# Kernel optimization log

Hardware: AMD Instinct MI355X
Metric: run time of the kernel (lower is better)

The kernel has to match this reference:

```python
import jax, jax.numpy as jnp
import numpy as np

B, S, D, H = 4, 2048, 2048, 16
HD = D // H  # 128
THETA = 10000.0


def setup_inputs() -> dict:
    key = jax.random.key(0)
    k1, k2, k3 = jax.random.split(key, 3)
    x = jax.random.normal(k1, (B, S, D), dtype=jnp.float32)
    wqkv = jax.random.normal(k2, (3 * D, D), dtype=jnp.float32) * (1.0 / np.sqrt(D))
    wo = jax.random.normal(k3, (D, D), dtype=jnp.float32) * (1.0 / np.sqrt(D))
    return {"x": x, "wqkv": wqkv, "wo": wo}


def _rotate_half(t):
    t1 = t[..., : t.shape[-1] // 2]
    t2 = t[..., t.shape[-1] // 2 :]
    return jnp.concatenate([-t2, t1], axis=-1)


def reference(x, wqkv, wo):
    b, s, d = x.shape
    h, hd = H, HD
    # fused QKV projection (Linear without bias: x @ W^T)
    qkv = jnp.einsum("bsd,ed->bse", x, wqkv).reshape(b, s, 3, h, hd)
    xq, xk, xv = qkv[:, :, 0], qkv[:, :, 1], qkv[:, :, 2]

    # RoPE tables (start_pos = 0)
    inv_freq = 1.0 / (THETA ** (jnp.arange(0, hd, 2, dtype=jnp.float32) / hd))
    t = jnp.arange(s, dtype=jnp.float32)
    freqs = jnp.outer(t, inv_freq)  # [s, hd/2]
    cos = jnp.concatenate([jnp.cos(freqs)] * 2, axis=-1).reshape(1, s, 1, hd)
    sin = jnp.concatenate([jnp.sin(freqs)] * 2, axis=-1).reshape(1, s, 1, hd)

    xq = xq * cos + _rotate_half(xq) * sin
    xk = xk * cos + _rotate_half(xk) * sin

    # causal SDPA (kv_cache is None, seq_len > 1)
    scale = 1.0 / np.sqrt(hd)
    scores = jnp.einsum("bqhd,bkhd->bhqk", xq, xk) * scale
    causal = jnp.tril(jnp.ones((s, s), dtype=bool))
    scores = jnp.where(causal, scores, jnp.finfo(scores.dtype).min)
    attn = jax.nn.softmax(scores, axis=-1)
    out = jnp.einsum("bhqk,bkhd->bqhd", attn, xv).reshape(b, s, d)
    return jnp.einsum("bsd,od->bso", out, wo)
```

## Files before the change

kernel.cpp:

```cpp
#include <hip/hip_runtime.h>

typedef unsigned short u16;
typedef unsigned int u32;
typedef __bf16 bf16x8 __attribute__((ext_vector_type(8)));
typedef float f32x4 __attribute__((ext_vector_type(4)));

#define S_LEN 2048
#define NH 16
#define HD 128

#define AS1 __attribute__((address_space(1)))
#define AS3 __attribute__((address_space(3)))

__device__ __forceinline__ u16 f2bf(float x) {
  u32 u = __builtin_bit_cast(u32, x);
  u32 r = u + 0x7FFFu + ((u >> 16) & 1u);
  return (u16)(r >> 16);
}
__device__ __forceinline__ float bf2f(u16 b) {
  return __builtin_bit_cast(float, (u32)b << 16);
}

__global__ void cvt_f32_bf16(const float* __restrict__ in, u16* __restrict__ out, int n4) {
  int i = blockIdx.x * 256 + threadIdx.x;
  if (i >= n4) return;
  float4 v = ((const float4*)in)[i];
  ushort4 o;
  o.x = f2bf(v.x); o.y = f2bf(v.y); o.z = f2bf(v.z); o.w = f2bf(v.w);
  ((ushort4*)out)[i] = o;
}

__global__ void build_tab(float* __restrict__ tab) {
  int t = blockIdx.x * 256 + threadIdx.x;
  int s = t >> 6, j = t & 63;
  float inv = exp2f(-(float)j * 0.20762050593045083f);
  float ang = (float)s * inv;
  tab[t] = cosf(ang);
  tab[131072 + t] = sinf(ang);
}

__device__ __forceinline__ void storeC(u16* p, float v) { *p = f2bf(v); }
__device__ __forceinline__ void storeC(float* p, float v) { *p = v; }

template <typename OutT>
__global__ __launch_bounds__(512, 2) void gemm_bt5(const u16* __restrict__ A, const u16* __restrict__ B,
                                                   OutT* __restrict__ C, int M, int N, int K, int nbx) {
  __shared__ alignas(16) u16 LDS[65536];
  char* lds = (char*)LDS;
  const int tid = threadIdx.x;
  const int lane = tid & 63;
  const int w = tid >> 6;
  const int wr = w >> 2, wc = w & 3;
  const int g = lane >> 4, c = lane & 15;

  const int nwg = gridDim.x;
  const int id = blockIdx.x;
  const int sw = (id & 7) * (nwg >> 3) + (id >> 3);
  const int bx = sw % nbx, by = sw / nbx;
  const size_t rowBase = (size_t)by * 256;
  const size_t colBase = (size_t)bx * 256;

  const int half = w & 1;
  const int sub = (w >> 1) & 3;
  const size_t ldb = (size_t)K * 2;
  const int srow = lane >> 3;
  const int soff = ((lane & 7) ^ srow) << 4;
  const char* ApS = (const char*)A + (rowBase + half * 128 + srow) * ldb + soff;
  const char* BpS = (const char*)B + (colBase + half * 128 + srow) * ldb + soff;

  auto stA = [&](int u, int blk) {
    const int r0 = blk * 32 + sub * 8;
    const int dst = ((u & 1) * 2 + half) * 16384 + r0 * 128;
    __builtin_amdgcn_global_load_lds((const AS1 void*)(ApS + (size_t)r0 * ldb + (size_t)u * 128),
                                     (AS3 void*)(lds + dst), 16, 0, 0);
  };
  auto stB = [&](int u, int jj) {
    const int r0 = (sub * 4 + jj) * 8;
    const int dst = 65536 + ((u & 1) * 2 + half) * 16384 + r0 * 128;
    __builtin_amdgcn_global_load_lds((const AS1 void*)(BpS + (size_t)r0 * ldb + (size_t)u * 128),
                                     (AS3 void*)(lds + dst), 16, 0, 0);
  };

  const int swz = (c & 7) << 4;
  auto rdA = [&](int bA, int mi, int kk) -> bf16x8 {
    return *(const bf16x8*)(lds + bA + mi * 2048 + c * 128 + ((kk * 64 + g * 16) ^ swz));
  };
  auto rdB = [&](int bB, int n, int kk) -> bf16x8 {
    return *(const bf16x8*)(lds + bB + n * 2048 + c * 128 + ((kk * 64 + g * 16) ^ swz));
  };

  f32x4 acc[8][4];
#pragma unroll
  for (int m = 0; m < 8; ++m)
#pragma unroll
    for (int n = 0; n < 4; ++n) acc[m][n] = f32x4{0.f, 0.f, 0.f, 0.f};

  bf16x8 bf_[4][2];
  auto mfmaPair = [&](int mi, bf16x8 ak0, bf16x8 ak1) {
#pragma unroll
    for (int n = 0; n < 4; ++n) {
      acc[mi][n] = __builtin_amdgcn_mfma_f32_16x16x32_bf16(ak0, bf_[n][0], acc[mi][n], 0, 0, 0);
      acc[mi][n] = __builtin_amdgcn_mfma_f32_16x16x32_bf16(ak1, bf_[n][1], acc[mi][n], 0, 0, 0);
    }
  };

  const int NT = K >> 6;

#pragma unroll
  for (int b = 0; b < 4; ++b) stA(0, b);
#pragma unroll
  for (int j = 0; j < 4; ++j) stB(0, j);
#pragma unroll
  for (int b = 0; b < 4; ++b) stA(1, b);
#pragma unroll
  for (int j = 0; j < 4; ++j) stB(1, j);
  asm volatile("s_waitcnt vmcnt(8)" ::: "memory");
  __builtin_amdgcn_s_barrier();

#pragma unroll 1
  for (int t = 0; t < NT; ++t) {
    const int bA = (t & 1) * 32768 + wr * 16384;
    const int bB = 65536 + (t & 1) * 32768 + (wc >> 1) * 16384 + (wc & 1) * 8192;
    bf16x8 a00, a01, a10, a11;
    a00 = rdA(bA, 0, 0); a01 = rdA(bA, 0, 1); a10 = rdA(bA, 1, 0); a11 = rdA(bA, 1, 1);
#pragma unroll
    for (int n = 0; n < 4; ++n) { bf_[n][0] = rdB(bB, n, 0); bf_[n][1] = rdB(bB, n, 1); }
    if (t >= 1 && t + 1 < NT) stA(t + 1, 3);
    __builtin_amdgcn_s_barrier();
    asm volatile("s_waitcnt lgkmcnt(0)" ::: "memory");
    __builtin_amdgcn_sched_barrier(0);
    __builtin_amdgcn_s_setprio(1);
    mfmaPair(0, a00, a01);
    mfmaPair(1, a10, a11);
    __builtin_amdgcn_s_setprio(0);
    __builtin_amdgcn_sched_barrier(0);
    __builtin_amdgcn_s_barrier();
    a00 = rdA(bA, 2, 0); a01 = rdA(bA, 2, 1); a10 = rdA(bA, 3, 0); a11 = rdA(bA, 3, 1);
    if (t + 2 < NT) { stA(t + 2, 0); stB(t + 2, 0); stB(t + 2, 1); }
    __builtin_amdgcn_s_barrier();
    asm volatile("s_waitcnt lgkmcnt(0)" ::: "memory");
    __builtin_amdgcn_sched_barrier(0);
    __builtin_amdgcn_s_setprio(1);
    mfmaPair(2, a00, a01);
    mfmaPair(3, a10, a11);
    __builtin_amdgcn_s_setprio(0);
    __builtin_amdgcn_sched_barrier(0);
    __builtin_amdgcn_s_barrier();
    a00 = rdA(bA, 4, 0); a01 = rdA(bA, 4, 1); a10 = rdA(bA, 5, 0); a11 = rdA(bA, 5, 1);
    if (t + 2 < NT) { stA(t + 2, 1); stB(t + 2, 2); stB(t + 2, 3); }
    __builtin_amdgcn_s_barrier();
    asm volatile("s_waitcnt lgkmcnt(0)" ::: "memory");
    __builtin_amdgcn_sched_barrier(0);
    __builtin_amdgcn_s_setprio(1);
    mfmaPair(4, a00, a01);
    mfmaPair(5, a10, a11);
    __builtin_amdgcn_s_setprio(0);
    __builtin_amdgcn_sched_barrier(0);
    __builtin_amdgcn_s_barrier();
    a00 = rdA(bA, 6, 0); a01 = rdA(bA, 6, 1); a10 = rdA(bA, 7, 0); a11 = rdA(bA, 7, 1);
    if (t + 2 < NT) stA(t + 2, 2);
    __builtin_amdgcn_s_barrier();
    asm volatile("s_waitcnt lgkmcnt(0)" ::: "memory");
    __builtin_amdgcn_sched_barrier(0);
    __builtin_amdgcn_s_setprio(1);
    mfmaPair(6, a00, a01);
    mfmaPair(7, a10, a11);
    __builtin_amdgcn_s_setprio(0);
    __builtin_amdgcn_sched_barrier(0);
    if (t + 2 < NT) { asm volatile("s_waitcnt vmcnt(7)" ::: "memory"); }
    else            { asm volatile("s_waitcnt vmcnt(0)" ::: "memory"); }
    __builtin_amdgcn_s_barrier();
  }

#pragma unroll
  for (int m = 0; m < 8; ++m)
#pragma unroll
    for (int n = 0; n < 4; ++n) {
      size_t row = rowBase + wr * 128 + m * 16 + g * 4;
      size_t col = colBase + wc * 64 + n * 16 + c;
#pragma unroll
      for (int r = 0; r < 4; ++r)
        storeC(&C[(row + r) * (size_t)N + col], acc[m][n][r]);
    }
}

__global__ void rope_qk(const u16* __restrict__ qkv, const float* __restrict__ tab,
                        u16* __restrict__ Q, u16* __restrict__ K) {
  int idx = blockIdx.x * 256 + threadIdx.x;
  int j = idx & 63;
  int s = (idx >> 6) & (S_LEN - 1);
  int h = (idx >> 17) & (NH - 1);
  int b = idx >> 21;
  float cs = tab[s * 64 + j];
  float sn = tab[131072 + s * 64 + j];
  size_t qbase = (((size_t)(b * S_LEN + s) * 3 + 0) * NH + h) * HD;
  size_t kbase = qbase + (size_t)NH * HD;
  size_t o = ((size_t)(b * NH + h) * S_LEN + s) * HD;
  float q1 = bf2f(qkv[qbase + j]),  q2 = bf2f(qkv[qbase + j + 64]);
  Q[o + j]      = f2bf(q1 * cs - q2 * sn);
  Q[o + j + 64] = f2bf(q2 * cs + q1 * sn);
  float k1 = bf2f(qkv[kbase + j]), k2 = bf2f(qkv[kbase + j + 64]);
  K[o + j]      = f2bf(k1 * cs - k2 * sn);
  K[o + j + 64] = f2bf(k2 * cs + k1 * sn);
}

__global__ void v_transpose(const u16* __restrict__ qkv, u16* __restrict__ Vt) {
  __shared__ u16 t[32][33];
  int bh = blockIdx.z;
  int s0 = blockIdx.x * 32;
  int d0 = blockIdx.y * 32;
  int b = bh >> 4, h = bh & 15;
  int col = threadIdx.x & 31;
  int row = threadIdx.x >> 5;
#pragma unroll
  for (int i = 0; i < 4; ++i) {
    int s = row + i * 8;
    t[s][col] = qkv[(((size_t)(b * S_LEN + s0 + s) * 3 + 2) * NH + h) * HD + d0 + col];
  }
  __syncthreads();
  size_t vb = ((size_t)bh * HD + d0) * S_LEN + s0;
#pragma unroll
  for (int i = 0; i < 4; ++i) {
    int d = row + i * 8;
    Vt[vb + (size_t)d * S_LEN + col] = t[col][d];
  }
}

__global__ __launch_bounds__(512, 4) void attn_fwd(const u16* __restrict__ Q, const u16* __restrict__ K,
                                                   const u16* __restrict__ Vt, u16* __restrict__ O) {
  __shared__ alignas(16) u16 Ks[2 * 64 * 128];
  __shared__ alignas(16) u16 Vs[2 * 128 * 64];
  __shared__ alignas(16) u16 Pl[8 * 16 * 64];
  const int tid = threadIdx.x;
  const int lane = tid & 63;
  const int w = tid >> 6;
  const int g = lane >> 4, c = lane & 15;
  const int bh = blockIdx.x;
  const int pair = blockIdx.y;
  const int b = bh >> 4, h = bh & 15;

  const u16* Qb = Q + (size_t)bh * S_LEN * HD;
  const u16* Kb = K + (size_t)bh * S_LEN * HD;
  const u16* Vb = Vt + (size_t)bh * HD * S_LEN;
  const float SL = 0.12751753f;
  const int swz = (c & 7) << 4;

  int ldsOff[2], srcK[2], srcV[2];
#pragma unroll
  for (int ii = 0; ii < 2; ++ii) {
    int p = (w * 2 + ii) * 1024 + lane * 16;
    ldsOff[ii] = p;
    int rk = p >> 8, ik = p & 255;
    srcK[ii] = rk * 256 + (ik ^ ((rk & 7) << 4));
    int rv = p >> 7, iv = p & 127;
    srcV[ii] = rv * (S_LEN * 2) + (iv ^ ((rv & 7) << 4));
  }
  int koff[4], voff[2];
#pragma unroll
  for (int kb = 0; kb < 4; ++kb) koff[kb] = (kb * 64 + g * 16) ^ swz;
  voff[0] = (g * 16) ^ swz;
  voff[1] = (64 + g * 16) ^ swz;
  int poff[4];
#pragma unroll
  for (int t = 0; t < 4; ++t) poff[t] = (t * 32 + g * 8) ^ swz;
  char* Pw = (char*)Pl + w * 2048;

#pragma unroll 1
  for (int ph = 0; ph < 2; ++ph) {
    const int sti = ph ? (15 - pair) : pair;
    const int qb0 = sti * 128;
    const int q0 = qb0 + w * 16;

    bf16x8 qf[4];
#pragma unroll
    for (int kb = 0; kb < 4; ++kb)
      qf[kb] = *(const bf16x8*)&Qb[(size_t)(q0 + c) * HD + kb * 32 + g * 8];

    f32x4 acc[8];
#pragma unroll
    for (int cb = 0; cb < 8; ++cb) acc[cb] = f32x4{0.f, 0.f, 0.f, 0.f};
    float m_i = -3e38f, l_i = 0.f;

    const int nsteps = sti * 2 + 2;
#pragma unroll
    for (int ii = 0; ii < 2; ++ii) {
      __builtin_amdgcn_global_load_lds((const AS1 void*)((const char*)Kb + srcK[ii]),
                                       (AS3 void*)((char*)Ks + ldsOff[ii] - lane * 16), 16, 0, 0);
      __builtin_amdgcn_global_load_lds((const AS1 void*)((const char*)Vb + srcV[ii]),
                                       (AS3 void*)((char*)Vs + ldsOff[ii] - lane * 16), 16, 0, 0);
    }
    __syncthreads();
    int cur = 0;

#pragma unroll 1
    for (int st = 0; st < nsteps; ++st) {
      const int kv0 = st << 6;
      if (st + 1 < nsteps) {
        const char* kbase = (const char*)Kb + (size_t)(kv0 + 64) * 256;
        const char* vbase = (const char*)Vb + (size_t)(kv0 + 64) * 2;
        const int nb = (cur ^ 1) * 16384;
#pragma unroll
        for (int ii = 0; ii < 2; ++ii) {
          __builtin_amdgcn_global_load_lds((const AS1 void*)(kbase + srcK[ii]),
                                           (AS3 void*)((char*)Ks + nb + ldsOff[ii] - lane * 16), 16, 0, 0);
          __builtin_amdgcn_global_load_lds((const AS1 void*)(vbase + srcV[ii]),
                                           (AS3 void*)((char*)Vs + nb + ldsOff[ii] - lane * 16), 16, 0, 0);
        }
      }
      if (kv0 < q0 + 16) {
        const char* Kt = (const char*)Ks + cur * 16384;
        const char* Vtl = (const char*)Vs + cur * 16384;
        f32x4 s[4];
#pragma unroll
        for (int t = 0; t < 4; ++t) s[t] = f32x4{0.f, 0.f, 0.f, 0.f};
#pragma unroll
        for (int t = 0; t < 4; ++t)
#pragma unroll
          for (int kb = 0; kb < 4; ++kb) {
            bf16x8 kf = *(const bf16x8*)(Kt + t * 4096 + c * 256 + koff[kb]);
            s[t] = __builtin_amdgcn_mfma_f32_16x16x32_bf16(kf, qf[kb], s[t], 0, 0, 0);
          }
        if (kv0 + 63 > q0) {
          const int lim = q0 + c - kv0 - 4 * g;
#pragma unroll
          for (int t = 0; t < 4; ++t)
#pragma unroll
            for (int r = 0; r < 4; ++r)
              s[t][r] = (16 * t + r <= lim) ? s[t][r] : -3e38f;
        }
        float mx = s[0][0];
#pragma unroll
        for (int t = 0; t < 4; ++t)
#pragma unroll
          for (int r = 0; r < 4; ++r) mx = fmaxf(mx, s[t][r]);
        mx = fmaxf(mx, __shfl_xor(mx, 16));
        mx = fmaxf(mx, __shfl_xor(mx, 32));
        const float mn = fmaxf(m_i, mx);
        const float alpha = exp2f((m_i - mn) * SL);
        float rs = 0.f;
#pragma unroll
        for (int t = 0; t < 4; ++t) {
          float p0 = exp2f((s[t][0] - mn) * SL);
          float p1 = exp2f((s[t][1] - mn) * SL);
          float p2 = exp2f((s[t][2] - mn) * SL);
          float p3 = exp2f((s[t][3] - mn) * SL);
          rs += (p0 + p1) + (p2 + p3);
          ushort4 pw;
          pw.x = f2bf(p0); pw.y = f2bf(p1); pw.z = f2bf(p2); pw.w = f2bf(p3);
          *(ushort4*)(Pw + c * 128 + poff[t]) = pw;
        }
        rs += __shfl_xor(rs, 16);
        rs += __shfl_xor(rs, 32);
        l_i = l_i * alpha + rs;
        m_i = mn;
        float ar[4];
#pragma unroll
        for (int r = 0; r < 4; ++r) ar[r] = __shfl(alpha, 4 * g + r);
#pragma unroll
        for (int cb = 0; cb < 8; ++cb)
#pragma unroll
          for (int r = 0; r < 4; ++r) acc[cb][r] *= ar[r];
        bf16x8 pa0 = *(const bf16x8*)(Pw + c * 128 + voff[0]);
        bf16x8 pa1 = *(const bf16x8*)(Pw + c * 128 + voff[1]);
#pragma unroll
        for (int cb = 0; cb < 8; ++cb) {
          bf16x8 vf0 = *(const bf16x8*)(Vtl + cb * 2048 + c * 128 + voff[0]);
          acc[cb] = __builtin_amdgcn_mfma_f32_16x16x32_bf16(pa0, vf0, acc[cb], 0, 0, 0);
          bf16x8 vf1 = *(const bf16x8*)(Vtl + cb * 2048 + c * 128 + voff[1]);
          acc[cb] = __builtin_amdgcn_mfma_f32_16x16x32_bf16(pa1, vf1, acc[cb], 0, 0, 0);
        }
      }
      __syncthreads();
      cur ^= 1;
    }
    float linv = 1.0f / l_i;
    float lr[4];
#pragma unroll
    for (int r = 0; r < 4; ++r) lr[r] = __shfl(linv, 4 * g + r);
#pragma unroll
    for (int cb = 0; cb < 8; ++cb)
#pragma unroll
      for (int r = 0; r < 4; ++r) {
        int q = q0 + 4 * g + r;
        O[(((size_t)b * S_LEN + q) * NH + h) * HD + cb * 16 + c] = f2bf(acc[cb][r] * lr[r]);
      }
  }
}

extern "C" void kernel_launch(void* const* d_in, const int* in_sizes, int n_in,
                              void* d_out, int out_size, void* d_ws, size_t ws_size,
                              hipStream_t stream) {
  const float* x    = (const float*)d_in[0];
  const float* wqkv = (const float*)d_in[1];
  const float* wo   = (const float*)d_in[2];
  float* out = (float*)d_out;
  char* ws = (char*)d_ws;

  u16*  xb    = (u16*)(ws + 0);
  u16*  wqkvb = (u16*)(ws + 33554432);
  float* tab  = (float*)(ws + 58720256);
  u16*  wob   = (u16*)(ws + 58720256);
  u16*  qkvb  = (u16*)(ws + 67108864);
  u16*  Vt    = (u16*)(ws + 167772160);
  u16*  attn  = (u16*)(ws + 0);
  u16*  Qr = (u16*)d_out;
  u16*  Kr = (u16*)d_out + 16777216;

  cvt_f32_bf16<<<16384, 256, 0, stream>>>(x, xb, 16777216 / 4);
  cvt_f32_bf16<<<12288, 256, 0, stream>>>(wqkv, wqkvb, 12582912 / 4);
  build_tab<<<512, 256, 0, stream>>>(tab);

  gemm_bt5<u16><<<768, 512, 0, stream>>>(xb, wqkvb, qkvb, 8192, 6144, 2048, 24);

  rope_qk<<<32768, 256, 0, stream>>>(qkvb, tab, Qr, Kr);
  v_transpose<<<dim3(64, 4, 64), 256, 0, stream>>>(qkvb, Vt);

  cvt_f32_bf16<<<4096, 256, 0, stream>>>(wo, wob, 4194304 / 4);

  attn_fwd<<<dim3(64, 8), 512, 0, stream>>>(Qr, Kr, Vt, attn);

  gemm_bt5<float><<<256, 512, 0, stream>>>(attn, wob, out, 8192, 2048, 2048, 8);
}
```

Measured before the change: 451.3 us.

## Double-buffer A fragments in registers to overlap LDS reads with MFMA

Restructures the GEMM inner loop so the A-operand LDS reads for the next pair of row-blocks are issued before the current MFMAs run, using two register sets (aP/aQ) and partial lgkmcnt waits. The first fragment set for the next K-tile is preloaded at the end of each iteration, and one barrier per phase is removed. This aims to hide LDS latency behind matrix work, at the cost of more VGPRs, which risks spills under the 512x2 launch bounds.

```diff
diff --git a/kernel.cpp b/kernel.cpp
--- a/kernel.cpp
+++ b/kernel.cpp
@@ -43,7 +43,7 @@
 __device__ __forceinline__ void storeC(float* p, float v) { *p = v; }
 
 template <typename OutT>
-__global__ __launch_bounds__(512, 2) void gemm_bt5(const u16* __restrict__ A, const u16* __restrict__ B,
+__global__ __launch_bounds__(512, 2) void gemm_bt6(const u16* __restrict__ A, const u16* __restrict__ B,
                                                    OutT* __restrict__ C, int M, int N, int K, int nbx) {
   __shared__ alignas(16) u16 LDS[65536];
   char* lds = (char*)LDS;
@@ -96,11 +96,24 @@
     for (int n = 0; n < 4; ++n) acc[m][n] = f32x4{0.f, 0.f, 0.f, 0.f};
 
   bf16x8 bf_[4][2];
-  auto mfmaPair = [&](int mi, bf16x8 ak0, bf16x8 ak1) {
+  bf16x8 aP[4], aQ[4];
+
+  auto loadA = [&](bf16x8 (&s)[4], int bA, int mi) {
+    s[0] = rdA(bA, mi, 0); s[1] = rdA(bA, mi, 1);
+    s[2] = rdA(bA, mi + 1, 0); s[3] = rdA(bA, mi + 1, 1);
+  };
+  auto loadR1 = [&](int bA, int bB) {
+    loadA(aP, bA, 0);
+#pragma unroll
+    for (int n = 0; n < 4; ++n) { bf_[n][0] = rdB(bB, n, 0); bf_[n][1] = rdB(bB, n, 1); }
+  };
+  auto MFMA2 = [&](int mi, bf16x8 (&s)[4]) {
 #pragma unroll
     for (int n = 0; n < 4; ++n) {
-      acc[mi][n] = __builtin_amdgcn_mfma_f32_16x16x32_bf16(ak0, bf_[n][0], acc[mi][n], 0, 0, 0);
-      acc[mi][n] = __builtin_amdgcn_mfma_f32_16x16x32_bf16(ak1, bf_[n][1], acc[mi][n], 0, 0, 0);
+      acc[mi][n]     = __builtin_amdgcn_mfma_f32_16x16x32_bf16(s[0], bf_[n][0], acc[mi][n], 0, 0, 0);
+      acc[mi][n]     = __builtin_amdgcn_mfma_f32_16x16x32_bf16(s[1], bf_[n][1], acc[mi][n], 0, 0, 0);
+      acc[mi + 1][n] = __builtin_amdgcn_mfma_f32_16x16x32_bf16(s[2], bf_[n][0], acc[mi + 1][n], 0, 0, 0);
+      acc[mi + 1][n] = __builtin_amdgcn_mfma_f32_16x16x32_bf16(s[3], bf_[n][1], acc[mi + 1][n], 0, 0, 0);
     }
   };
 
@@ -116,60 +129,58 @@
   for (int j = 0; j < 4; ++j) stB(1, j);
   asm volatile("s_waitcnt vmcnt(8)" ::: "memory");
   __builtin_amdgcn_s_barrier();
+  {
+    const int bA0 = wr * 16384;
+    const int bB0 = 65536 + (wc >> 1) * 16384 + (wc & 1) * 8192;
+    loadR1(bA0, bB0);
+  }
 
 #pragma unroll 1
   for (int t = 0; t < NT; ++t) {
     const int bA = (t & 1) * 32768 + wr * 16384;
     const int bB = 65536 + (t & 1) * 32768 + (wc >> 1) * 16384 + (wc & 1) * 8192;
-    bf16x8 a00, a01, a10, a11;
-    a00 = rdA(bA, 0, 0); a01 = rdA(bA, 0, 1); a10 = rdA(bA, 1, 0); a11 = rdA(bA, 1, 1);
-#pragma unroll
-    for (int n = 0; n < 4; ++n) { bf_[n][0] = rdB(bB, n, 0); bf_[n][1] = rdB(bB, n, 1); }
+    loadA(aQ, bA, 2);
     if (t >= 1 && t + 1 < NT) stA(t + 1, 3);
+    asm volatile("s_waitcnt lgkmcnt(4)" ::: "memory");
+    __builtin_amdgcn_sched_barrier(0);
+    __builtin_amdgcn_s_setprio(1);
+    MFMA2(0, aP);
+    __builtin_amdgcn_s_setprio(0);
+    __builtin_amdgcn_sched_barrier(0);
     __builtin_amdgcn_s_barrier();
+    loadA(aP, bA, 4);
+    if (t + 2 < NT) { stA(t + 2, 0); stB(t + 2, 0); stB(t + 2, 1); }
+    asm volatile("s_waitcnt lgkmcnt(4)" ::: "memory");
+    __builtin_amdgcn_sched_barrier(0);
+    __builtin_amdgcn_s_setprio(1);
+    MFMA2(2, aQ);
+    __builtin_amdgcn_s_setprio(0);
+    __builtin_amdgcn_sched_barrier(0);
+    __builtin_amdgcn_s_barrier();
+    loadA(aQ, bA, 6);
+    if (t + 2 < NT) { stA(t + 2, 1); stB(t + 2, 2); stB(t + 2, 3); }
+    asm volatile("s_waitcnt lgkmcnt(4)" ::: "memory");
+    __builtin_amdgcn_sched_barrier(0);
+    __builtin_amdgcn_s_setprio(1);
+    MFMA2(4, aP);
+    __builtin_amdgcn_s_setprio(0);
+    __builtin_amdgcn_sched_barrier(0);
+    __builtin_amdgcn_s_barrier();
+    if (t + 2 < NT) stA(t + 2, 2);
     asm volatile("s_waitcnt lgkmcnt(0)" ::: "memory");
     __builtin_amdgcn_sched_barrier(0);
     __builtin_amdgcn_s_setprio(1);
-    mfmaPair(0, a00, a01);
-    mfmaPair(1, a10, a11);
-    __builtin_amdgcn_s_setprio(0);
-    __builtin_amdgcn_sched_barrier(0);
-    __builtin_amdgcn_s_barrier();
-    a00 = rdA(bA, 2, 0); a01 = rdA(bA, 2, 1); a10 = rdA(bA, 3, 0); a11 = rdA(bA, 3, 1);
-    if (t + 2 < NT) { stA(t + 2, 0); stB(t + 2, 0); stB(t + 2, 1); }
-    __builtin_amdgcn_s_barrier();
-    asm volatile("s_waitcnt lgkmcnt(0)" ::: "memory");
-    __builtin_amdgcn_sched_barrier(0);
-    __builtin_amdgcn_s_setprio(1);
-    mfmaPair(2, a00, a01);
-    mfmaPair(3, a10, a11);
-    __builtin_amdgcn_s_setprio(0);
-    __builtin_amdgcn_sched_barrier(0);
-    __builtin_amdgcn_s_barrier();
-    a00 = rdA(bA, 4, 0); a01 = rdA(bA, 4, 1); a10 = rdA(bA, 5, 0); a11 = rdA(bA, 5, 1);
-    if (t + 2 < NT) { stA(t + 2, 1); stB(t + 2, 2); stB(t + 2, 3); }
-    __builtin_amdgcn_s_barrier();
-    asm volatile("s_waitcnt lgkmcnt(0)" ::: "memory");
-    __builtin_amdgcn_sched_barrier(0);
-    __builtin_amdgcn_s_setprio(1);
-    mfmaPair(4, a00, a01);
-    mfmaPair(5, a10, a11);
-    __builtin_amdgcn_s_setprio(0);
-    __builtin_amdgcn_sched_barrier(0);
-    __builtin_amdgcn_s_barrier();
-    a00 = rdA(bA, 6, 0); a01 = rdA(bA, 6, 1); a10 = rdA(bA, 7, 0); a11 = rdA(bA, 7, 1);
-    if (t + 2 < NT) stA(t + 2, 2);
-    __builtin_amdgcn_s_barrier();
-    asm volatile("s_waitcnt lgkmcnt(0)" ::: "memory");
-    __builtin_amdgcn_sched_barrier(0);
-    __builtin_amdgcn_s_setprio(1);
-    mfmaPair(6, a00, a01);
-    mfmaPair(7, a10, a11);
+    MFMA2(6, aQ);
     __builtin_amdgcn_s_setprio(0);
     __builtin_amdgcn_sched_barrier(0);
     if (t + 2 < NT) { asm volatile("s_waitcnt vmcnt(7)" ::: "memory"); }
     else            { asm volatile("s_waitcnt vmcnt(0)" ::: "memory"); }
     __builtin_amdgcn_s_barrier();
+    if (t + 1 < NT) {
+      const int bA1 = ((t + 1) & 1) * 32768 + wr * 16384;
+      const int bB1 = 65536 + ((t + 1) & 1) * 32768 + (wc >> 1) * 16384 + (wc & 1) * 8192;
+      loadR1(bA1, bB1);
+    }
   }
 
 #pragma unroll
@@ -410,7 +421,7 @@
   cvt_f32_bf16<<<12288, 256, 0, stream>>>(wqkv, wqkvb, 12582912 / 4);
   build_tab<<<512, 256, 0, stream>>>(tab);
 
-  gemm_bt5<u16><<<768, 512, 0, stream>>>(xb, wqkvb, qkvb, 8192, 6144, 2048, 24);
+  gemm_bt6<u16><<<768, 512, 0, stream>>>(xb, wqkvb, qkvb, 8192, 6144, 2048, 24);
 
   rope_qk<<<32768, 256, 0, stream>>>(qkvb, tab, Qr, Kr);
   v_transpose<<<dim3(64, 4, 64), 256, 0, stream>>>(qkvb, Vt);
@@ -419,5 +430,5 @@
 
   attn_fwd<<<dim3(64, 8), 512, 0, stream>>>(Qr, Kr, Vt, attn);
 
-  gemm_bt5<float><<<256, 512, 0, stream>>>(attn, wob, out, 8192, 2048, 2048, 8);
-}
+  gemm_bt6<float><<<256, 512, 0, stream>>>(attn, wob, out, 8192, 2048, 2048, 8);
+}
```

New measurement: 434.2 us. -3.8%, faster.
